# Optimization experiments

Measured on AMD Instinct MI355X. Metric: run time of the kernel, lower is better.

Reference implementation:

```python
import jax, jax.numpy as jnp
import numpy as np

EPS = 1e-4  # F.normalize eps


def setup_inputs() -> dict:
    key = jax.random.key(0)
    k1, k2, k3, k4 = jax.random.split(key, 4)
    return {
        "pred_feat": jax.random.normal(k1, (8192, 6), dtype=jnp.float32),
        "pred_decoder": jax.random.normal(k2, (4096, 4), dtype=jnp.float32),
        "input_data": jax.random.normal(k3, (4096, 4), dtype=jnp.float32),
        "gt_data": jax.random.normal(k4, (32768, 6), dtype=jnp.float32),
    }


def _normalize(x, eps=EPS):
    # torch F.normalize: x / max(||x||, eps)
    n = jnp.linalg.norm(x, axis=1, keepdims=True)
    return x / jnp.maximum(n, eps)


def reference(pred_feat, pred_decoder, input_data, gt_data):
    # train_decoder=False path (default inference/encoder-training path)
    pred_points = pred_feat[:, :3]    # [N,3]
    pred_normals = pred_feat[:, 3:]   # [N,3]
    gt_points = gt_data[:, :3]        # [L,3]
    gt_normals = gt_data[:, 3:]       # [L,3]

    # Squared Euclidean distances; argmin over squared == argmin over cdist(p=2).
    # dists2: [N, L] -- the big memory-bound intermediate
    p2 = jnp.sum(pred_points * pred_points, axis=1, keepdims=True)   # [N,1]
    g2 = jnp.sum(gt_points * gt_points, axis=1)                       # [L]
    dists2 = p2 - 2.0 * (pred_points @ gt_points.T) + g2[None, :]
    min_indices = jnp.argmin(dists2, axis=1)                          # [N]

    matched_pts = gt_points[min_indices]                              # [N,3]
    inlier_loss = jnp.mean((pred_points - matched_pts) ** 2)

    matched_nrm = gt_normals[min_indices]                             # [N,3]
    cos_theta = jnp.sum(_normalize(pred_normals) * _normalize(matched_nrm), axis=1)
    norm_loss = jnp.mean(1.0 - cos_theta)

    return inlier_loss + norm_loss
```

## Files before the change

### kernel.cpp

```cpp
#include <hip/hip_runtime.h>
#include <float.h>

#define NPRED 8192
#define NGT   32768
#define BLK   256
#define P     4
#define NCHUNK (NPRED / (BLK * P))
#define NSEG   128
#define SEGLEN (NGT / NSEG)
#define G      8
#define NGRP   (SEGLEN / G)
#define FBLK   256
#define NPB    (NPRED / FBLK)


__global__ void prep_kernel(const float* __restrict__ gt, float4* __restrict__ gt4,
                            unsigned long long* __restrict__ res,
                            unsigned int* __restrict__ counter) {
    int j = blockIdx.x * blockDim.x + threadIdx.x;
    if (j < NGT) {
        float x = gt[j * 6 + 0], y = gt[j * 6 + 1], z = gt[j * 6 + 2];
        gt4[j] = make_float4(-2.0f * x, -2.0f * y, -2.0f * z, x * x + y * y + z * z);
    }
    if (j < NPRED) res[j] = 0xFFFFFFFFFFFFFFFFull;
    if (j == 0) *counter = 0u;
}

__device__ __forceinline__ unsigned int fkey(float f) {
    unsigned int u = __float_as_uint(f);
    return u ^ (unsigned int)(((int)u >> 31) | 0x80000000);
}

__device__ __forceinline__ float score(const float4& g, float px, float py, float pz) {
    return fmaf(g.x, px, fmaf(g.y, py, fmaf(g.z, pz, g.w)));
}

__global__ __launch_bounds__(BLK, 4) void argmin_kernel(const float* __restrict__ pred,
                                                        const float4* __restrict__ gt4,
                                                        unsigned long long* __restrict__ res) {
    __shared__ float4 tile[SEGLEN];
    const int t = threadIdx.x;
    const int chunk = blockIdx.x;
    const int seg = blockIdx.y;
    const int j0 = seg * SEGLEN;

    tile[t] = gt4[j0 + t];

    float px[P], py[P], pz[P], best[P];
    int bg[P];
    const int pbase = chunk * (BLK * P) + t;
    #pragma unroll
    for (int k = 0; k < P; ++k) {
        const float* p = pred + (size_t)(pbase + k * BLK) * 6;
        px[k] = p[0]; py[k] = p[1]; pz[k] = p[2];
        best[k] = FLT_MAX; bg[k] = 0;
    }
    __syncthreads();

    #pragma unroll 1
    for (int grp = 0; grp < NGRP; ++grp) {
        const int base = grp * G;
        float4 g0 = tile[base + 0], g1 = tile[base + 1];
        float4 g2 = tile[base + 2], g3 = tile[base + 3];
        float4 g4 = tile[base + 4], g5 = tile[base + 5];
        float4 g6 = tile[base + 6], g7 = tile[base + 7];
        #pragma unroll
        for (int k = 0; k < P; ++k) {
            float s0 = score(g0, px[k], py[k], pz[k]);
            float s1 = score(g1, px[k], py[k], pz[k]);
            float s2 = score(g2, px[k], py[k], pz[k]);
            float s3 = score(g3, px[k], py[k], pz[k]);
            float s4 = score(g4, px[k], py[k], pz[k]);
            float s5 = score(g5, px[k], py[k], pz[k]);
            float s6 = score(g6, px[k], py[k], pz[k]);
            float s7 = score(g7, px[k], py[k], pz[k]);
            float t0 = fminf(fminf(s0, s1), s2);
            float t1 = fminf(fminf(s3, s4), s5);
            float t2 = fminf(fminf(s6, s7), t0);
            float m  = fminf(t1, t2);
            if (m < best[k]) { best[k] = m; bg[k] = grp; }
        }
    }

    #pragma unroll
    for (int k = 0; k < P; ++k) {
        const int gb = bg[k] * G;
        float s[G];
        #pragma unroll
        for (int o = 0; o < G; ++o)
            s[o] = score(tile[gb + o], px[k], py[k], pz[k]);
        int off = G - 1;
        #pragma unroll
        for (int o = G - 2; o >= 0; --o)
            if (s[o] == best[k]) off = o;
        unsigned long long pk = ((unsigned long long)fkey(best[k]) << 32)
                              | (unsigned long long)(j0 + gb + off);
        atomicMin(&res[pbase + k * BLK], pk);
    }
}

__global__ __launch_bounds__(FBLK) void finalize_kernel(const float* __restrict__ pred,
                                                        const float* __restrict__ gt,
                                                        const unsigned long long* __restrict__ res,
                                                        unsigned long long* __restrict__ bsums,
                                                        unsigned int* __restrict__ counter,
                                                        float* __restrict__ out) {
    int i = blockIdx.x * FBLK + threadIdx.x;
    int bidx = (int)(res[i] & 0xFFFFFFFFull);

    const float* g = &gt[(size_t)bidx * 6];
    float gx = g[0], gy = g[1], gz = g[2];
    float gnx = g[3], gny = g[4], gnz = g[5];
    const float* p = &pred[(size_t)i * 6];
    float px = p[0], py = p[1], pz = p[2];
    float pnx = p[3], pny = p[4], pnz = p[5];

    float dx = px - gx, dy = py - gy, dz = pz - gz;
    float v1 = dx * dx + dy * dy + dz * dz;

    float pn = sqrtf(pnx * pnx + pny * pny + pnz * pnz);
    float gn = sqrtf(gnx * gnx + gny * gny + gnz * gnz);
    float denom = fmaxf(pn, 1e-4f) * fmaxf(gn, 1e-4f);
    float cosv = (pnx * gnx + pny * gny + pnz * gnz) / denom;
    float v2 = 1.0f - cosv;

    #pragma unroll
    for (int off = 32; off > 0; off >>= 1) {
        v1 += __shfl_down(v1, off);
        v2 += __shfl_down(v2, off);
    }
    __shared__ float s1[FBLK / 64];
    __shared__ float s2[FBLK / 64];
    __shared__ int lastFlag;
    int wid = threadIdx.x >> 6;
    if ((threadIdx.x & 63) == 0) { s1[wid] = v1; s2[wid] = v2; }
    __syncthreads();
    if (threadIdx.x == 0) {
        float a = 0.0f, b = 0.0f;
        #pragma unroll
        for (int w = 0; w < FBLK / 64; ++w) { a += s1[w]; b += s2[w]; }
        unsigned long long pk = (unsigned long long)__float_as_uint(a)
                              | ((unsigned long long)__float_as_uint(b) << 32);
        __hip_atomic_store(&bsums[blockIdx.x], pk, __ATOMIC_RELEASE, __HIP_MEMORY_SCOPE_AGENT);
        unsigned int tk = __hip_atomic_fetch_add(counter, 1u, __ATOMIC_ACQ_REL, __HIP_MEMORY_SCOPE_AGENT);
        lastFlag = (tk == NPB - 1) ? 1 : 0;
    }
    __syncthreads();
    if (lastFlag && threadIdx.x < 64) {
        float a = 0.0f, b = 0.0f;
        if (threadIdx.x < NPB) {
            unsigned long long pk = __hip_atomic_load(&bsums[threadIdx.x],
                                                      __ATOMIC_ACQUIRE, __HIP_MEMORY_SCOPE_AGENT);
            a = __uint_as_float((unsigned int)(pk & 0xFFFFFFFFull));
            b = __uint_as_float((unsigned int)(pk >> 32));
        }
        #pragma unroll
        for (int off = 32; off > 0; off >>= 1) {
            a += __shfl_down(a, off);
            b += __shfl_down(b, off);
        }
        if (threadIdx.x == 0) out[0] = a / (NPRED * 3.0f) + b / (float)NPRED;
    }
}

extern "C" void kernel_launch(void* const* d_in, const int* in_sizes, int n_in,
                              void* d_out, int out_size, void* d_ws, size_t ws_size,
                              hipStream_t stream) {
    const float* pred_feat = (const float*)d_in[0];
    const float* gt_data   = (const float*)d_in[3];
    float* out = (float*)d_out;

    char* ws = (char*)d_ws;
    float4* gt4 = (float4*)ws;
    unsigned long long* res = (unsigned long long*)(ws + (size_t)NGT * 16);
    unsigned long long* bsums = (unsigned long long*)(ws + (size_t)NGT * 16 + (size_t)NPRED * 8);
    unsigned int* counter = (unsigned int*)(ws + (size_t)NGT * 16 + (size_t)NPRED * 8 + (size_t)NPB * 8);

    prep_kernel<<<NGT / 256, 256, 0, stream>>>(gt_data, gt4, res, counter);
    dim3 grid(NCHUNK, NSEG);
    argmin_kernel<<<grid, BLK, 0, stream>>>(pred_feat, gt4, res);
    finalize_kernel<<<NPB, FBLK, 0, stream>>>(pred_feat, gt_data, res, bsums, counter, out);
}
```

Baseline: 39.26 us.

## Fuse gt prep into argmin, replace atomicMin with per-segment partials reduced in finalize

Removes the separate prep kernel: each argmin block now transforms its own gt segment into the shared tile. Global 64-bit atomicMin is replaced by writing per-segment packed keys to a partial buffer, and finalize reduces the 256 partials per point. P goes from 4 to 8 and NSEG from 128 to 256, which keeps the grid at 1024 blocks with 128-entry segments, and the group loop is unrolled by 2. The counter reset moves into the argmin kernel. This trades one kernel launch and atomic contention for a 16 MB partial buffer that finalize must read, plus higher register pressure from P=8.

```diff
diff --git a/kernel.cpp b/kernel.cpp
--- a/kernel.cpp
+++ b/kernel.cpp
@@ -4,27 +4,15 @@
 #define NPRED 8192
 #define NGT   32768
 #define BLK   256
-#define P     4
+#define P     8
+#define NSEG  256
+#define SEGLEN (NGT / NSEG)
 #define NCHUNK (NPRED / (BLK * P))
-#define NSEG   128
-#define SEGLEN (NGT / NSEG)
 #define G      8
 #define NGRP   (SEGLEN / G)
 #define FBLK   256
 #define NPB    (NPRED / FBLK)
 
-
-__global__ void prep_kernel(const float* __restrict__ gt, float4* __restrict__ gt4,
-                            unsigned long long* __restrict__ res,
-                            unsigned int* __restrict__ counter) {
-    int j = blockIdx.x * blockDim.x + threadIdx.x;
-    if (j < NGT) {
-        float x = gt[j * 6 + 0], y = gt[j * 6 + 1], z = gt[j * 6 + 2];
-        gt4[j] = make_float4(-2.0f * x, -2.0f * y, -2.0f * z, x * x + y * y + z * z);
-    }
-    if (j < NPRED) res[j] = 0xFFFFFFFFFFFFFFFFull;
-    if (j == 0) *counter = 0u;
-}
 
 __device__ __forceinline__ unsigned int fkey(float f) {
     unsigned int u = __float_as_uint(f);
@@ -36,15 +24,22 @@
 }
 
 __global__ __launch_bounds__(BLK, 4) void argmin_kernel(const float* __restrict__ pred,
-                                                        const float4* __restrict__ gt4,
-                                                        unsigned long long* __restrict__ res) {
+                                                        const float* __restrict__ gt,
+                                                        unsigned long long* __restrict__ part,
+                                                        unsigned int* __restrict__ counter) {
     __shared__ float4 tile[SEGLEN];
     const int t = threadIdx.x;
     const int chunk = blockIdx.x;
     const int seg = blockIdx.y;
     const int j0 = seg * SEGLEN;
 
-    tile[t] = gt4[j0 + t];
+    if (chunk == 0 && seg == 0 && t == 0) *counter = 0u;
+
+    if (t < SEGLEN) {
+        const float* g = gt + (size_t)(j0 + t) * 6;
+        float x = g[0], y = g[1], z = g[2];
+        tile[t] = make_float4(-2.0f * x, -2.0f * y, -2.0f * z, x * x + y * y + z * z);
+    }
 
     float px[P], py[P], pz[P], best[P];
     int bg[P];
@@ -57,7 +52,7 @@
     }
     __syncthreads();
 
-    #pragma unroll 1
+    #pragma unroll 2
     for (int grp = 0; grp < NGRP; ++grp) {
         const int base = grp * G;
         float4 g0 = tile[base + 0], g1 = tile[base + 1];
@@ -95,18 +90,25 @@
             if (s[o] == best[k]) off = o;
         unsigned long long pk = ((unsigned long long)fkey(best[k]) << 32)
                               | (unsigned long long)(j0 + gb + off);
-        atomicMin(&res[pbase + k * BLK], pk);
+        part[(size_t)seg * NPRED + pbase + k * BLK] = pk;
     }
 }
 
 __global__ __launch_bounds__(FBLK) void finalize_kernel(const float* __restrict__ pred,
                                                         const float* __restrict__ gt,
-                                                        const unsigned long long* __restrict__ res,
+                                                        const unsigned long long* __restrict__ part,
                                                         unsigned long long* __restrict__ bsums,
                                                         unsigned int* __restrict__ counter,
                                                         float* __restrict__ out) {
     int i = blockIdx.x * FBLK + threadIdx.x;
-    int bidx = (int)(res[i] & 0xFFFFFFFFull);
+
+    unsigned long long cur = 0xFFFFFFFFFFFFFFFFull;
+    #pragma unroll 4
+    for (int s = 0; s < NSEG; ++s) {
+        unsigned long long k = part[(size_t)s * NPRED + i];
+        cur = (k < cur) ? k : cur;
+    }
+    int bidx = (int)(cur & 0xFFFFFFFFull);
 
     const float* g = &gt[(size_t)bidx * 6];
     float gx = g[0], gy = g[1], gz = g[2];
@@ -171,13 +173,11 @@
     float* out = (float*)d_out;
 
     char* ws = (char*)d_ws;
-    float4* gt4 = (float4*)ws;
-    unsigned long long* res = (unsigned long long*)(ws + (size_t)NGT * 16);
-    unsigned long long* bsums = (unsigned long long*)(ws + (size_t)NGT * 16 + (size_t)NPRED * 8);
-    unsigned int* counter = (unsigned int*)(ws + (size_t)NGT * 16 + (size_t)NPRED * 8 + (size_t)NPB * 8);
+    unsigned long long* part  = (unsigned long long*)ws;
+    unsigned long long* bsums = (unsigned long long*)(ws + (size_t)NSEG * NPRED * 8);
+    unsigned int* counter     = (unsigned int*)(ws + (size_t)NSEG * NPRED * 8 + (size_t)NPB * 8);
 
-    prep_kernel<<<NGT / 256, 256, 0, stream>>>(gt_data, gt4, res, counter);
     dim3 grid(NCHUNK, NSEG);
-    argmin_kernel<<<grid, BLK, 0, stream>>>(pred_feat, gt4, res);
-    finalize_kernel<<<NPB, FBLK, 0, stream>>>(pred_feat, gt_data, res, bsums, counter, out);
+    argmin_kernel<<<grid, BLK, 0, stream>>>(pred_feat, gt_data, part, counter);
+    finalize_kernel<<<NPB, FBLK, 0, stream>>>(pred_feat, gt_data, part, bsums, counter, out);
 }
```

Result: slower. 60.40 us (+53.8%).
